# Kernel tuning notes

Hardware: AMD Instinct MI355X
Metric: run time of the kernel (lower is better)

## Reference

```python
import jax, jax.numpy as jnp
import numpy as np

_B, _Q, _D, _H, _L, _F, _C, _HM = 8, 100, 256, 8, 9, 2048, 151, 112


def setup_inputs():
    key = jax.random.key(0)
    ks = list(jax.random.split(key, 40)); ki = [0]
    def nk():
        k = ks[ki[0]]; ki[0] += 1; return k
    def r(shape, s=1.0):
        return jax.random.normal(nk(), shape, jnp.float32) * s
    z, o = jnp.zeros, jnp.ones
    return {
        'mask_features': r((_B, _D, _HM, _HM)),
        'mem0': r((_B, _D, 14, 14)), 'mem1': r((_B, _D, 28, 28)), 'mem2': r((_B, _D, 56, 56)),
        'query_feat': r((_Q, _D), 0.02), 'query_embed': r((_Q, _D), 0.02),
        'ca_wqkv': r((_L, 3, _D, _D), 0.02), 'ca_bqkv': z((_L, 3, _D)),
        'ca_wo': r((_L, _D, _D), 0.02), 'ca_bo': z((_L, _D)),
        'ca_ln_s': o((_L, _D)), 'ca_ln_b': z((_L, _D)),
        'sa_wqkv': r((_L, 3, _D, _D), 0.02), 'sa_bqkv': z((_L, 3, _D)),
        'sa_wo': r((_L, _D, _D), 0.02), 'sa_bo': z((_L, _D)),
        'sa_ln_s': o((_L, _D)), 'sa_ln_b': z((_L, _D)),
        'ffn_w1': r((_L, _D, _F), 0.02), 'ffn_b1': z((_L, _F)),
        'ffn_w2': r((_L, _F, _D), 0.02), 'ffn_b2': z((_L, _D)),
        'ffn_ln_s': o((_L, _D)), 'ffn_ln_b': z((_L, _D)),
        'dec_ln_s': o((_D,)), 'dec_ln_b': z((_D,)),
        'me_w1': r((_D, _D), 0.02), 'me_b1': z((_D,)),
        'me_w2': r((_D, _D), 0.02), 'me_b2': z((_D,)),
        'me_w3': r((_D, _D), 0.02), 'me_b3': z((_D,)),
        'cls_w': r((_D, _C), 0.02), 'cls_b': z((_C,)),
    }


def _ln(x, s, b, eps=1e-5):
    m = x.mean(-1, keepdims=True)
    v = ((x - m) ** 2).mean(-1, keepdims=True)
    return (x - m) * jax.lax.rsqrt(v + eps) * s + b


def _mha(q, k, v, wqkv, bqkv, wo, bo, bias):
    # q: [B,Nq,D]; k,v: [B,Nk,D]; bias: [B,1,Nq,Nk] additive (-1e9 = masked) or None
    B, Nq, D = q.shape
    hd = D // _H
    qh = (q @ wqkv[0] + bqkv[0]).reshape(B, Nq, _H, hd)
    kh = (k @ wqkv[1] + bqkv[1]).reshape(B, -1, _H, hd)
    vh = (v @ wqkv[2] + bqkv[2]).reshape(B, -1, _H, hd)
    scores = jnp.einsum('bqhd,bkhd->bhqk', qh, kh) / np.sqrt(hd).astype(np.float32)
    if bias is not None:
        scores = scores + bias
    attn = jax.nn.softmax(scores, axis=-1)
    out = jnp.einsum('bhqk,bkhd->bqhd', attn, vh).reshape(B, Nq, D)
    return out @ wo + bo


def _attn_bias(prev_mask, hw):
    # prev_mask: [B,Q,Hm,Wm] raw logits -> additive bias [B,1,Q,H*W]
    B, Q = prev_mask.shape[:2]
    r = jax.image.resize(prev_mask, (B, Q) + hw, 'bilinear')  # align_corners=False
    ignore = (jax.nn.sigmoid(r) < 0.5).reshape(B, Q, -1)      # True = masked out
    fully = jnp.all(ignore, axis=-1, keepdims=True)           # un-mask fully-masked rows
    ignore = jnp.where(fully, False, ignore)
    return jnp.where(ignore, jnp.float32(-1e9), jnp.float32(0.0))[:, None]


def _forward(mask_features, mem0, mem1, mem2, query_feat, query_embed,
             ca_wqkv, ca_bqkv, ca_wo, ca_bo, ca_ln_s, ca_ln_b,
             sa_wqkv, sa_bqkv, sa_wo, sa_bo, sa_ln_s, sa_ln_b,
             ffn_w1, ffn_b1, ffn_w2, ffn_b2, ffn_ln_s, ffn_ln_b,
             dec_ln_s, dec_ln_b, me_w1, me_b1, me_w2, me_b2, me_w3, me_b3,
             cls_w, cls_b):
    B, D, Hm, Wm = mask_features.shape
    Q = query_feat.shape[0]
    mems = [(m.reshape(B, D, -1).transpose(0, 2, 1), m.shape[2:]) for m in (mem0, mem1, mem2)]
    mask_flat = mask_features.reshape(B, D, -1).transpose(0, 2, 1)  # [B,Hm*Wm,D]
    q = jnp.broadcast_to((query_feat + query_embed)[None], (B, Q, D))
    prev = None
    for i in range(_L):
        mem, hw = mems[i % 3]
        bias = _attn_bias(prev, hw) if prev is not None else None
        q = _ln(q + _mha(q, mem, mem, ca_wqkv[i], ca_bqkv[i], ca_wo[i], ca_bo[i], bias), ca_ln_s[i], ca_ln_b[i])
        q = _ln(q + _mha(q, q, q, sa_wqkv[i], sa_bqkv[i], sa_wo[i], sa_bo[i], None), sa_ln_s[i], sa_ln_b[i])
        h = jax.nn.relu(q @ ffn_w1[i] + ffn_b1[i]) @ ffn_w2[i] + ffn_b2[i]
        q = _ln(q + h, ffn_ln_s[i], ffn_ln_b[i])
        nq = _ln(q, dec_ln_s, dec_ln_b)
        me = jax.nn.relu(jax.nn.relu(nq @ me_w1 + me_b1) @ me_w2 + me_b2) @ me_w3 + me_b3
        pred_mask = jnp.einsum('bqd,bpd->bqp', me, mask_flat).reshape(B, Q, Hm, Wm)
        prev = jax.lax.stop_gradient(pred_mask)
    pred_logits = nq @ cls_w + cls_b
    return pred_logits, pred_mask


def reference(mask_features, mem0, mem1, mem2, query_feat, query_embed,
              ca_wqkv, ca_bqkv, ca_wo, ca_bo, ca_ln_s, ca_ln_b,
              sa_wqkv, sa_bqkv, sa_wo, sa_bo, sa_ln_s, sa_ln_b,
              ffn_w1, ffn_b1, ffn_w2, ffn_b2, ffn_ln_s, ffn_ln_b,
              dec_ln_s, dec_ln_b, me_w1, me_b1, me_w2, me_b2, me_w3, me_b3,
              cls_w, cls_b):
    return _forward(mask_features, mem0, mem1, mem2, query_feat, query_embed,
                    ca_wqkv, ca_bqkv, ca_wo, ca_bo, ca_ln_s, ca_ln_b,
                    sa_wqkv, sa_bqkv, sa_wo, sa_bo, sa_ln_s, sa_ln_b,
                    ffn_w1, ffn_b1, ffn_w2, ffn_b2, ffn_ln_s, ffn_ln_b,
                    dec_ln_s, dec_ln_b, me_w1, me_b1, me_w2, me_b2, me_w3, me_b3,
                    cls_w, cls_b)
```

## Files before the change

kernel.cpp:

```cpp
#include <hip/hip_runtime.h>
#include <cmath>

#define B_ 8
#define Q_ 100
#define D_ 256
#define H_ 8
#define HD_ 32
#define L_ 9
#define F_ 2048
#define C_ 151
#define HM_ 112
#define PMAX_ 3136
#define KT_ 128
#define RECSZ 544

typedef __attribute__((ext_vector_type(4))) short s4v;
typedef __attribute__((ext_vector_type(8))) short s8v;
typedef __attribute__((ext_vector_type(4))) float f4v;

__device__ __forceinline__ unsigned short f2bf(float x) {
  unsigned int u = __float_as_uint(x);
  return (unsigned short)((u + 0x7fffu + ((u >> 16) & 1u)) >> 16);
}
__device__ __forceinline__ float bf2f(unsigned short h) {
  return __uint_as_float(((unsigned int)h) << 16);
}
__device__ __forceinline__ void split2(float x, short& h, short& l) {
  unsigned short hb = f2bf(x);
  float r = x - bf2f(hb);
  h = (short)hb;
  l = (short)f2bf(r);
}

__device__ __forceinline__ float block_sum(float v, float* red) {
  int t = threadIdx.x;
  red[t] = v; __syncthreads();
  for (int s = 128; s > 0; s >>= 1) {
    if (t < s) red[t] += red[t + s];
    __syncthreads();
  }
  float r = red[0]; __syncthreads();
  return r;
}

__global__ __launch_bounds__(256) void initq_kernel(const float* __restrict__ qf,
                                                    const float* __restrict__ qe,
                                                    float* __restrict__ q) {
  int idx = blockIdx.x * 256 + threadIdx.x;
  int qd = idx % (Q_ * D_);
  q[idx] = qf[qd] + qe[qd];
}

__global__ __launch_bounds__(256) void tsplit_kernel(
    const float* __restrict__ in, short* __restrict__ out,
    int K, int N, long long ibs, long long obs) {
  __shared__ float tile[32][33];
  const int z = blockIdx.z;
  const int nb = blockIdx.x * 32, kb = blockIdx.y * 32;
  const float* I = in + (size_t)z * ibs;
  short* O = out + (size_t)z * obs;
  const int t = threadIdx.x;
  {
    const int r = t >> 3, c = (t & 7) * 4;
    const int gk = kb + r;
#pragma unroll
    for (int j = 0; j < 4; ++j) {
      int gn = nb + c + j;
      tile[r][c + j] = (gk < K && gn < N) ? I[(size_t)gk * N + gn] : 0.f;
    }
  }
  __syncthreads();
  {
    const int nr = t >> 3, kc = (t & 7) * 4;
    const int gn = nb + nr;
    if (gn < N) {
#pragma unroll
      for (int j = 0; j < 4; ++j) {
        int gk = kb + kc + j;
        if (gk < K) {
          short h, l; split2(tile[kc + j][nr], h, l);
          O[(size_t)gn * 2 * K + gk] = h;
          O[(size_t)gn * 2 * K + K + gk] = l;
        }
      }
    }
  }
}

__device__ __forceinline__ s8v ldfrag(const short* p) {
  s4v lo = *(const s4v*)p;
  s4v hi = *(const s4v*)(p + 16);
  return __builtin_shufflevector(lo, hi, 0, 1, 2, 3, 4, 5, 6, 7);
}

template <int BM, int AMODE, int WMODE, bool RELU, int OUT>
__global__ __launch_bounds__(256) void mgemm_kernel(
    const void* __restrict__ Ap, const void* __restrict__ Wp,
    const float* __restrict__ bias, void* __restrict__ Cv,
    int M, int N, int K,
    long long Abs, long long Wbs, long long Cbs, int ldc, int swap) {
  constexpr int MI = BM / 32;
  __shared__ short Ah[BM * 36], Al[BM * 36], Wh[128 * 36], Wl[128 * 36];
  const int z = blockIdx.z;
  const int bx = swap ? blockIdx.y : blockIdx.x;
  const int by = swap ? blockIdx.x : blockIdx.y;
  const int n0 = bx * 128, m0 = by * BM;
  const int t = threadIdx.x;
  const int lane = t & 63;
  const int wave = t >> 6;
  const int wm = wave >> 1, wn = wave & 1;
  const int lr = lane & 15, lg = lane >> 4;
  f4v acc[MI][4];
#pragma unroll
  for (int i = 0; i < MI; ++i)
#pragma unroll
    for (int j = 0; j < 4; ++j) acc[i][j] = (f4v){0.f, 0.f, 0.f, 0.f};

  for (int k0 = 0; k0 < K; k0 += 32) {
    if (AMODE == 0) {
      const float* A = (const float*)Ap + (size_t)z * Abs;
      if (BM == 64) {
        const int arow = t >> 2;
        const int kc = (t & 3) * 8;
        float x[8];
        if (m0 + arow < M) {
          const float* ap = A + (size_t)(m0 + arow) * K + k0 + kc;
          *(f4v*)&x[0] = *(const f4v*)ap;
          *(f4v*)&x[4] = *(const f4v*)(ap + 4);
        } else {
#pragma unroll
          for (int e = 0; e < 8; ++e) x[e] = 0.f;
        }
        s4v h0, h1, l0, l1;
#pragma unroll
        for (int e = 0; e < 4; ++e) { short hh, ll; split2(x[e], hh, ll); h0[e] = hh; l0[e] = ll; }
#pragma unroll
        for (int e = 0; e < 4; ++e) { short hh, ll; split2(x[4 + e], hh, ll); h1[e] = hh; l1[e] = ll; }
        *(s4v*)&Ah[arow * 36 + kc] = h0; *(s4v*)&Ah[arow * 36 + kc + 4] = h1;
        *(s4v*)&Al[arow * 36 + kc] = l0; *(s4v*)&Al[arow * 36 + kc + 4] = l1;
      } else {
        const int arow = t >> 3;
        const int kc = (t & 7) * 4;
        float x[4];
        if (m0 + arow < M) {
          *(f4v*)&x[0] = *(const f4v*)(A + (size_t)(m0 + arow) * K + k0 + kc);
        } else {
#pragma unroll
          for (int e = 0; e < 4; ++e) x[e] = 0.f;
        }
        s4v h0, l0;
#pragma unroll
        for (int e = 0; e < 4; ++e) { short hh, ll; split2(x[e], hh, ll); h0[e] = hh; l0[e] = ll; }
        *(s4v*)&Ah[arow * 36 + kc] = h0;
        *(s4v*)&Al[arow * 36 + kc] = l0;
      }
    } else {
      const short* A2 = (const short*)Ap + (size_t)z * Abs;
      const int arow = t >> 2;
      const int c = t & 3, sel = c >> 1, ko = (c & 1) * 16;
      s8v v0 = {0, 0, 0, 0, 0, 0, 0, 0}, v1 = {0, 0, 0, 0, 0, 0, 0, 0};
      if (m0 + arow < M) {
        const short* ap = A2 + (size_t)(m0 + arow) * (2 * K) + sel * K + k0 + ko;
        v0 = *(const s8v*)ap;
        v1 = *(const s8v*)(ap + 8);
      }
      short* dst = sel ? Al : Ah;
      *(s4v*)&dst[arow * 36 + ko] = __builtin_shufflevector(v0, v0, 0, 1, 2, 3);
      *(s4v*)&dst[arow * 36 + ko + 4] = __builtin_shufflevector(v0, v0, 4, 5, 6, 7);
      *(s4v*)&dst[arow * 36 + ko + 8] = __builtin_shufflevector(v1, v1, 0, 1, 2, 3);
      *(s4v*)&dst[arow * 36 + ko + 12] = __builtin_shufflevector(v1, v1, 4, 5, 6, 7);
    }
    if (WMODE == 0) {
      const short* W2 = (const short*)Wp + (size_t)z * Wbs;
      const int n = t >> 1, sel = t & 1;
      const short* wp = W2 + (size_t)(n0 + n) * (2 * K) + sel * K + k0;
      short* dst = sel ? Wl : Wh;
#pragma unroll
      for (int j = 0; j < 4; ++j) {
        s8v v = *(const s8v*)(wp + j * 8);
        *(s4v*)&dst[n * 36 + j * 8] = __builtin_shufflevector(v, v, 0, 1, 2, 3);
        *(s4v*)&dst[n * 36 + j * 8 + 4] = __builtin_shufflevector(v, v, 4, 5, 6, 7);
      }
    } else {
      const float* W = (const float*)Wp + (size_t)z * Wbs;
      const int kr = t >> 3, c0 = (t & 7) * 16;
      const float* wp = W + (size_t)(k0 + kr) * N + n0 + c0;
      float x[16];
#pragma unroll
      for (int j = 0; j < 4; ++j) *(f4v*)&x[j * 4] = *(const f4v*)(wp + j * 4);
#pragma unroll
      for (int j = 0; j < 16; ++j) {
        short hh, ll; split2(x[j], hh, ll);
        Wh[(c0 + j) * 36 + kr] = hh;
        Wl[(c0 + j) * 36 + kr] = ll;
      }
    }
    __syncthreads();
    s8v whf[4], wlf[4];
#pragma unroll
    for (int ni = 0; ni < 4; ++ni) {
      whf[ni] = ldfrag(&Wh[(wn * 64 + ni * 16 + lr) * 36 + 4 * lg]);
      wlf[ni] = ldfrag(&Wl[(wn * 64 + ni * 16 + lr) * 36 + 4 * lg]);
    }
#pragma unroll
    for (int mi = 0; mi < MI; ++mi) {
      s8v ah = ldfrag(&Ah[(wm * (BM / 2) + mi * 16 + lr) * 36 + 4 * lg]);
      s8v al = ldfrag(&Al[(wm * (BM / 2) + mi * 16 + lr) * 36 + 4 * lg]);
#pragma unroll
      for (int ni = 0; ni < 4; ++ni) {
        acc[mi][ni] = __builtin_amdgcn_mfma_f32_16x16x32_bf16(ah, whf[ni], acc[mi][ni], 0, 0, 0);
        acc[mi][ni] = __builtin_amdgcn_mfma_f32_16x16x32_bf16(al, whf[ni], acc[mi][ni], 0, 0, 0);
        acc[mi][ni] = __builtin_amdgcn_mfma_f32_16x16x32_bf16(ah, wlf[ni], acc[mi][ni], 0, 0, 0);
      }
    }
    __syncthreads();
  }
  float* Cf = (float*)Cv + (size_t)z * Cbs;
  unsigned short* Ch = (unsigned short*)Cv + (size_t)z * Cbs;
#pragma unroll
  for (int mi = 0; mi < MI; ++mi) {
#pragma unroll
    for (int i = 0; i < 4; ++i) {
      int row = m0 + wm * (BM / 2) + mi * 16 + 4 * lg + i;
      if (row >= M) continue;
#pragma unroll
      for (int ni = 0; ni < 4; ++ni) {
        int col = n0 + wn * 64 + ni * 16 + lr;
        float v = acc[mi][ni][i] + (bias ? bias[col] : 0.f);
        if (RELU) v = fmaxf(v, 0.f);
        if (OUT == 0) Cf[(size_t)row * ldc + col] = v;
        else Ch[(size_t)row * ldc + col] = f2bf(v);
      }
    }
  }
}

__global__ __launch_bounds__(256) void maskhead_kernel(
    const float* __restrict__ q, const float* __restrict__ lns,
    const float* __restrict__ lnb, const short* __restrict__ W123,
    const float* __restrict__ b1, const float* __restrict__ b2,
    const float* __restrict__ b3,
    float* __restrict__ nqout, float* __restrict__ me3out) {
  __shared__ float Xb[16 * 264], Yb[16 * 264];
  __shared__ short Ah[16 * 36], Al[16 * 36], Wh[256 * 36], Wl[256 * 36];
  const int r0 = blockIdx.x * 16;
  const int t = threadIdx.x;
  const int lane = t & 63, w = t >> 6;
  const int lr = lane & 15, lg = lane >> 4;
#pragma unroll
  for (int rr = 0; rr < 4; ++rr) {
    int row = w * 4 + rr;
    int grow = r0 + row;
    f4v v = *((const f4v*)(q + (size_t)grow * D_) + lane);
    float sum = v[0] + v[1] + v[2] + v[3];
#pragma unroll
    for (int off = 32; off > 0; off >>= 1) sum += __shfl_xor(sum, off, 64);
    float mean = sum * (1.f / D_);
    float c0 = v[0] - mean, c1 = v[1] - mean, c2 = v[2] - mean, c3 = v[3] - mean;
    float vs = c0 * c0 + c1 * c1 + c2 * c2 + c3 * c3;
#pragma unroll
    for (int off = 32; off > 0; off >>= 1) vs += __shfl_xor(vs, off, 64);
    float inv = rsqrtf(vs * (1.f / D_) + 1e-5f);
    f4v sv = *((const f4v*)lns + lane);
    f4v bv = *((const f4v*)lnb + lane);
    f4v o;
    o[0] = c0 * inv * sv[0] + bv[0];
    o[1] = c1 * inv * sv[1] + bv[1];
    o[2] = c2 * inv * sv[2] + bv[2];
    o[3] = c3 * inv * sv[3] + bv[3];
    *(f4v*)&Xb[row * 264 + lane * 4] = o;
    *((f4v*)(nqout + (size_t)grow * D_) + lane) = o;
  }
  __syncthreads();
  float* src = Xb;
  float* dst = Yb;
  for (int s = 0; s < 3; ++s) {
    const short* Ws = W123 + (size_t)s * 131072;
    const float* bs = (s == 0) ? b1 : ((s == 1) ? b2 : b3);
    f4v acc[4];
#pragma unroll
    for (int j = 0; j < 4; ++j) acc[j] = (f4v){0.f, 0.f, 0.f, 0.f};
    for (int k0 = 0; k0 < 256; k0 += 32) {
      {
        int idx = t * 2;
        int row = idx >> 5, kc = idx & 31;
        short h0, l0, h1, l1;
        split2(src[row * 264 + k0 + kc], h0, l0);
        split2(src[row * 264 + k0 + kc + 1], h1, l1);
        Ah[row * 36 + kc] = h0; Ah[row * 36 + kc + 1] = h1;
        Al[row * 36 + kc] = l0; Al[row * 36 + kc + 1] = l1;
      }
      {
        const short* wp = Ws + (size_t)t * 512 + k0;
#pragma unroll
        for (int j = 0; j < 8; ++j)
          *(s4v*)&Wh[t * 36 + j * 4] = *(const s4v*)(wp + j * 4);
        const short* wpl = wp + 256;
#pragma unroll
        for (int j = 0; j < 8; ++j)
          *(s4v*)&Wl[t * 36 + j * 4] = *(const s4v*)(wpl + j * 4);
      }
      __syncthreads();
      s8v ah = ldfrag(&Ah[lr * 36 + 4 * lg]);
      s8v al = ldfrag(&Al[lr * 36 + 4 * lg]);
#pragma unroll
      for (int ni = 0; ni < 4; ++ni) {
        s8v wh = ldfrag(&Wh[(w * 64 + ni * 16 + lr) * 36 + 4 * lg]);
        s8v wl = ldfrag(&Wl[(w * 64 + ni * 16 + lr) * 36 + 4 * lg]);
        acc[ni] = __builtin_amdgcn_mfma_f32_16x16x32_bf16(ah, wh, acc[ni], 0, 0, 0);
        acc[ni] = __builtin_amdgcn_mfma_f32_16x16x32_bf16(al, wh, acc[ni], 0, 0, 0);
        acc[ni] = __builtin_amdgcn_mfma_f32_16x16x32_bf16(ah, wl, acc[ni], 0, 0, 0);
      }
      __syncthreads();
    }
#pragma unroll
    for (int ni = 0; ni < 4; ++ni) {
#pragma unroll
      for (int i = 0; i < 4; ++i) {
        int row = 4 * lg + i;
        int col = w * 64 + ni * 16 + lr;
        float v = acc[ni][i] + bs[col];
        if (s < 2) v = fmaxf(v, 0.f);
        dst[row * 264 + col] = v;
      }
    }
    __syncthreads();
    float* tmpp = src; src = dst; dst = tmpp;
  }
  for (int o = t; o < 16 * 256; o += 256) {
    int row = o >> 8, col = o & 255;
    me3out[(size_t)(r0 + row) * D_ + col] = src[row * 264 + col];
  }
}

__global__ __launch_bounds__(256) void gemm32_kernel(
    const float* __restrict__ A, const float* __restrict__ W,
    const float* __restrict__ bias, float* __restrict__ C,
    int M, int N, int K) {
  __shared__ float As[16][65];
  __shared__ float Ws[16][65];
  const int n0 = blockIdx.x * 64, m0 = blockIdx.y * 64;
  const int t = threadIdx.x;
  const int tm = t >> 4, tn = t & 15;
  float acc[4][4] = {};
  for (int k0 = 0; k0 < K; k0 += 16) {
#pragma unroll
    for (int l = 0; l < 4; ++l) {
      int idx = t + l * 256;
      int am = idx >> 4, ak = idx & 15;
      int gm = m0 + am, gk = k0 + ak;
      As[ak][am] = (gm < M) ? A[(size_t)gm * K + gk] : 0.f;
      int wk = idx >> 6, wn = idx & 63;
      int gn = n0 + wn, gk2 = k0 + wk;
      Ws[wk][wn] = (gn < N) ? W[(size_t)gk2 * N + gn] : 0.f;
    }
    __syncthreads();
#pragma unroll
    for (int kk = 0; kk < 16; ++kk) {
      float a[4], b[4];
#pragma unroll
      for (int i = 0; i < 4; ++i) a[i] = As[kk][tm * 4 + i];
#pragma unroll
      for (int j = 0; j < 4; ++j) b[j] = Ws[kk][tn * 4 + j];
#pragma unroll
      for (int i = 0; i < 4; ++i)
#pragma unroll
        for (int j = 0; j < 4; ++j) acc[i][j] += a[i] * b[j];
    }
    __syncthreads();
  }
#pragma unroll
  for (int i = 0; i < 4; ++i) {
    int gm = m0 + tm * 4 + i;
    if (gm >= M) continue;
#pragma unroll
    for (int j = 0; j < 4; ++j) {
      int gn = n0 + tn * 4 + j;
      if (gn >= N) continue;
      C[(size_t)gm * N + gn] = acc[i][j] + bias[gn];
    }
  }
}

template <bool RES>
__global__ __launch_bounds__(256) void ln_kernel(const float* __restrict__ x,
                                                 const float* __restrict__ r,
                                                 const float* __restrict__ s,
                                                 const float* __restrict__ b,
                                                 float* __restrict__ out, int nrows) {
  const int wave = threadIdx.x >> 6, lane = threadIdx.x & 63;
  const int row = blockIdx.x * 4 + wave;
  if (row >= nrows) return;
  f4v v = *((const f4v*)(x + (size_t)row * D_) + lane);
  if (RES) {
    f4v rv = *((const f4v*)(r + (size_t)row * D_) + lane);
    v[0] += rv[0]; v[1] += rv[1]; v[2] += rv[2]; v[3] += rv[3];
  }
  float sum = v[0] + v[1] + v[2] + v[3];
#pragma unroll
  for (int off = 32; off > 0; off >>= 1) sum += __shfl_xor(sum, off, 64);
  float mean = sum * (1.f / D_);
  float c0 = v[0] - mean, c1 = v[1] - mean, c2 = v[2] - mean, c3 = v[3] - mean;
  float vs = c0 * c0 + c1 * c1 + c2 * c2 + c3 * c3;
#pragma unroll
  for (int off = 32; off > 0; off >>= 1) vs += __shfl_xor(vs, off, 64);
  float inv = rsqrtf(vs * (1.f / D_) + 1e-5f);
  f4v sv = *((const f4v*)s + lane);
  f4v bv = *((const f4v*)b + lane);
  f4v o;
  o[0] = c0 * inv * sv[0] + bv[0];
  o[1] = c1 * inv * sv[1] + bv[1];
  o[2] = c2 * inv * sv[2] + bv[2];
  o[3] = c3 * inv * sv[3] + bv[3];
  *((f4v*)(out + (size_t)row * D_) + lane) = o;
}

template <bool BIAS, bool KVBF16, bool SPLIT>
__global__ __launch_bounds__(256) void mattn_kernel(
    const float* __restrict__ qb, int ldq,
    const void* __restrict__ kbv, int ldk,
    const void* __restrict__ vbv, int ldv,
    const unsigned int* __restrict__ bits,
    float* __restrict__ outp, int P, int Pw, int tps, int S) {
  __shared__ __align__(16) short Kt[128 * 40];
  __shared__ __align__(16) short Vt[32 * 132];
  __shared__ __align__(16) short Pt[4 * 16 * 36];
  __shared__ unsigned int bb[64];
  __shared__ float Msh[4][16], Lsh[4][16];
  float* Osh = (float*)Kt;
  const int b = blockIdx.x >> 3, h = blockIdx.x & 7;
  const int q0 = blockIdx.y * 16;
  const int seg = blockIdx.z;
  const int kbeg = seg * tps * KT_;
  const int kend = min(P, kbeg + tps * KT_);
  const int t = threadIdx.x;
  const int lane = t & 63, w = t >> 6;
  const int lr = lane & 15, lg = lane >> 4;
  const float scale = 0.17677669529663687f;

  s8v qhf, qlf;
  {
    int qrow = q0 + lr; if (qrow >= Q_) qrow = Q_ - 1;
    const float* qp = qb + (size_t)(b * Q_ + qrow) * ldq + h * HD_;
#pragma unroll
    for (int e = 0; e < 8; ++e) {
      int d = 4 * lg + (e & 3) + 16 * (e >> 2);
      short hh, ll; split2(qp[d], hh, ll);
      qhf[e] = hh; qlf[e] = ll;
    }
  }
  float mreg[4], lreg[4];
  f4v accO0 = (f4v){0.f, 0.f, 0.f, 0.f}, accO1 = (f4v){0.f, 0.f, 0.f, 0.f};
#pragma unroll
  for (int i = 0; i < 4; ++i) { mreg[i] = -3.0e38f; lreg[i] = 0.f; }

  for (int k0 = kbeg; k0 < kend; k0 += KT_) {
    {
      const int key = t >> 1, dh = (t & 1) * 16;
      const int gk = k0 + key;
      s8v ka = {0,0,0,0,0,0,0,0}, kb2 = {0,0,0,0,0,0,0,0};
      s8v va = {0,0,0,0,0,0,0,0}, vb2 = {0,0,0,0,0,0,0,0};
      if (gk < kend) {
        if (KVBF16) {
          const unsigned short* kp = (const unsigned short*)kbv + (size_t)(b * P + gk) * ldk + h * HD_ + dh;
          const unsigned short* vp = (const unsigned short*)vbv + (size_t)(b * P + gk) * ldv + h * HD_ + dh;
          ka = *(const s8v*)kp; kb2 = *(const s8v*)(kp + 8);
          va = *(const s8v*)vp; vb2 = *(const s8v*)(vp + 8);
        } else {
          const float* kp = (const float*)kbv + (size_t)(b * P + gk) * ldk + h * HD_ + dh;
          const float* vp = (const float*)vbv + (size_t)(b * P + gk) * ldv + h * HD_ + dh;
#pragma unroll
          for (int j = 0; j < 8; ++j) {
            ka[j] = (short)f2bf(kp[j]); kb2[j] = (short)f2bf(kp[8 + j]);
            va[j] = (short)f2bf(vp[j]); vb2[j] = (short)f2bf(vp[8 + j]);
          }
        }
      }
      *(s8v*)&Kt[key * 40 + dh] = ka;
      *(s8v*)&Kt[key * 40 + dh + 8] = kb2;
#pragma unroll
      for (int j = 0; j < 8; ++j) {
        Vt[(dh + j) * 132 + key] = va[j];
        Vt[(dh + 8 + j) * 132 + key] = vb2[j];
      }
    }
    if (BIAS && t < 64) {
      int qq = t >> 2, wi = t & 3;
      int gr = q0 + qq, gw = (k0 >> 5) + wi;
      bb[t] = (gr < Q_ && gw < Pw) ? bits[(size_t)(b * Q_ + gr) * Pw + gw] : 0u;
    }
    __syncthreads();
    s8v kf0 = ldfrag(&Kt[(w * 32 + lr) * 40 + 4 * lg]);
    s8v kf1 = ldfrag(&Kt[(w * 32 + 16 + lr) * 40 + 4 * lg]);
    f4v accS0 = (f4v){0.f, 0.f, 0.f, 0.f}, accS1 = (f4v){0.f, 0.f, 0.f, 0.f};
    accS0 = __builtin_amdgcn_mfma_f32_16x16x32_bf16(qhf, kf0, accS0, 0, 0, 0);
    accS0 = __builtin_amdgcn_mfma_f32_16x16x32_bf16(qlf, kf0, accS0, 0, 0, 0);
    accS1 = __builtin_amdgcn_mfma_f32_16x16x32_bf16(qhf, kf1, accS1, 0, 0, 0);
    accS1 = __builtin_amdgcn_mfma_f32_16x16x32_bf16(qlf, kf1, accS1, 0, 0, 0);
    const int gk0 = k0 + w * 32 + lr;
#pragma unroll
    for (int i = 0; i < 4; ++i) {
      float s0 = accS0[i] * scale, s1 = accS1[i] * scale;
      if (BIAS) {
        unsigned int word = bb[(4 * lg + i) * 4 + w];
        if ((word >> lr) & 1u) s0 += -1e9f;
        if ((word >> (16 + lr)) & 1u) s1 += -1e9f;
      }
      if (gk0 >= kend) s0 = -3.0e38f;
      if (gk0 + 16 >= kend) s1 = -3.0e38f;
      float rm = fmaxf(s0, s1);
#pragma unroll
      for (int off = 1; off < 16; off <<= 1) rm = fmaxf(rm, __shfl_xor(rm, off, 64));
      float mn = fmaxf(mreg[i], rm);
      float corr = __expf(mreg[i] - mn);
      mreg[i] = mn;
      float p0 = __expf(s0 - mn), p1 = __expf(s1 - mn);
      lreg[i] = lreg[i] * corr + p0 + p1;
      accO0[i] *= corr;
      accO1[i] *= corr;
      Pt[w * 576 + (4 * lg + i) * 36 + lr] = (short)f2bf(p0);
      Pt[w * 576 + (4 * lg + i) * 36 + 16 + lr] = (short)f2bf(p1);
    }
    s8v pf = ldfrag(&Pt[w * 576 + lr * 36 + 4 * lg]);
    s8v vf0 = ldfrag(&Vt[lr * 132 + w * 32 + 4 * lg]);
    s8v vf1 = ldfrag(&Vt[(16 + lr) * 132 + w * 32 + 4 * lg]);
    accO0 = __builtin_amdgcn_mfma_f32_16x16x32_bf16(pf, vf0, accO0, 0, 0, 0);
    accO1 = __builtin_amdgcn_mfma_f32_16x16x32_bf16(pf, vf1, accO1, 0, 0, 0);
    __syncthreads();
  }
#pragma unroll
  for (int i = 0; i < 4; ++i) {
    float lv = lreg[i];
#pragma unroll
    for (int off = 1; off < 16; off <<= 1) lv += __shfl_xor(lv, off, 64);
    if (lr == 0) { Msh[w][4 * lg + i] = mreg[i]; Lsh[w][4 * lg + i] = lv; }
  }
#pragma unroll
  for (int i = 0; i < 4; ++i) {
    Osh[w * 528 + (4 * lg + i) * 33 + lr] = accO0[i];
    Osh[w * 528 + (4 * lg + i) * 33 + 16 + lr] = accO1[i];
  }
  __syncthreads();
  float* part = SPLIT
      ? outp + ((size_t)((blockIdx.x * gridDim.y + blockIdx.y) * S + seg)) * RECSZ
      : nullptr;
  for (int o = t; o < 512; o += 256) {
    int qq = o >> 5, d = o & 31;
    float M = fmaxf(fmaxf(Msh[0][qq], Msh[1][qq]), fmaxf(Msh[2][qq], Msh[3][qq]));
    float lt = 0.f, Ov = 0.f;
#pragma unroll
    for (int w4 = 0; w4 < 4; ++w4) {
      float wt = __expf(Msh[w4][qq] - M);
      lt += wt * Lsh[w4][qq];
      Ov += wt * Osh[w4 * 528 + qq * 33 + d];
    }
    if (SPLIT) {
      if (d == 0) { part[qq] = M; part[16 + qq] = lt; }
      part[32 + qq * 32 + d] = Ov;
    } else if (q0 + qq < Q_) {
      outp[(size_t)(b * Q_ + q0 + qq) * D_ + h * HD_ + d] = Ov / lt;
    }
  }
}

__global__ __launch_bounds__(256) void attncomb_kernel(
    const float* __restrict__ part, float* __restrict__ out, int S, int nqt) {
  const int row = blockIdx.x;
  const int b = row / Q_, qq = row % Q_;
  const int t = threadIdx.x;
  const int h = t >> 5, d = t & 31;
  const int qt = qq >> 4, r = qq & 15;
  const float* base = part + ((size_t)((b * 8 + h) * nqt + qt) * S) * RECSZ;
  float M = -3.0e38f;
  for (int s = 0; s < S; ++s) M = fmaxf(M, base[(size_t)s * RECSZ + r]);
  float lt = 0.f, Ov = 0.f;
  for (int s = 0; s < S; ++s) {
    const float* rec = base + (size_t)s * RECSZ;
    float w = __expf(rec[r] - M);
    lt += w * rec[16 + r];
    Ov += w * rec[32 + r * 32 + d];
  }
  out[(size_t)row * D_ + h * HD_ + d] = Ov / lt;
}

__global__ __launch_bounds__(256) void maskbias_kernel(
    const float* __restrict__ prev,
    unsigned int* __restrict__ bias,
    int oh) {
  __shared__ float pm[HM_ * HM_];
  __shared__ float rbuf[PMAX_];
  __shared__ float red[256];
  __shared__ unsigned int bw[128];
  const int row = blockIdx.x;
  const int t = threadIdx.x;
  const float* src = prev + (size_t)row * (HM_ * HM_);
  for (int i = t; i < HM_ * HM_; i += 256) pm[i] = src[i];
  __syncthreads();
  const int ratio = HM_ / oh;
  const int taps = 2 * ratio;
  const float invr = 1.f / (float)ratio;
  const int P = oh * oh;
  const int Pw = (P + 31) >> 5;
  float nign = 0.f;
  for (int p = t; p < P; p += 256) {
    int oy = p / oh, ox = p - oy * oh;
    float sy = (oy + 0.5f) * ratio - 0.5f;
    float sx = (ox + 0.5f) * ratio - 0.5f;
    int y0 = (int)floorf(sy - ratio) + 1;
    int x0 = (int)floorf(sx - ratio) + 1;
    float wxs = 0.f;
    for (int si = 0; si < taps; ++si) {
      int x = x0 + si;
      if (x < 0 || x >= HM_) continue;
      wxs += 1.f - fabsf(sx - x) * invr;
    }
    float acc = 0.f, wys = 0.f;
    for (int ti = 0; ti < taps; ++ti) {
      int y = y0 + ti;
      if (y < 0 || y >= HM_) continue;
      float wy = 1.f - fabsf(sy - y) * invr;
      wys += wy;
      float ra = 0.f;
      const float* pr = pm + y * HM_;
      for (int si = 0; si < taps; ++si) {
        int x = x0 + si;
        if (x < 0 || x >= HM_) continue;
        float wx = 1.f - fabsf(sx - x) * invr;
        ra += wx * pr[x];
      }
      acc += wy * ra;
    }
    float rv = acc / (wys * wxs);
    rbuf[p] = rv;
    if (!(rv < 0.f)) nign += 1.f;
  }
  float tot = block_sum(nign, red);
  bool fully = (tot == 0.f);
  for (int w = t; w < Pw; w += 256) bw[w] = 0u;
  __syncthreads();
  if (!fully) {
    for (int p = t; p < P; p += 256) {
      if (rbuf[p] < 0.f) atomicOr(&bw[p >> 5], 1u << (p & 31));
    }
  }
  __syncthreads();
  unsigned int* dst = bias + (size_t)row * Pw;
  for (int w = t; w < Pw; w += 256) dst[w] = bw[w];
}

static inline void mg(hipStream_t st, int bm, int amode, int wmode, bool relu,
                      const void* A, const void* W, const float* bias, void* C,
                      int M, int N, int K, int Z,
                      long long Abs, long long Wbs, long long Cbs, int ldc) {
  dim3 g(N / 128, (M + bm - 1) / bm, Z);
  if (bm == 32) {
    if (relu)
      mgemm_kernel<32, 0, 0, true, 0><<<g, 256, 0, st>>>(A, W, bias, C, M, N, K, Abs, Wbs, Cbs, ldc, 0);
    else
      mgemm_kernel<32, 0, 0, false, 0><<<g, 256, 0, st>>>(A, W, bias, C, M, N, K, Abs, Wbs, Cbs, ldc, 0);
  } else {
    if (amode == 1)
      mgemm_kernel<64, 1, 0, false, 1><<<g, 256, 0, st>>>(A, W, bias, C, M, N, K, Abs, Wbs, Cbs, ldc, 0);
    else
      mgemm_kernel<64, 0, 0, false, 0><<<g, 256, 0, st>>>(A, W, bias, C, M, N, K, Abs, Wbs, Cbs, ldc, 0);
  }
}

extern "C" void kernel_launch(void* const* d_in, const int* in_sizes, int n_in,
                              void* d_out, int out_size, void* d_ws, size_t ws_size,
                              hipStream_t stream) {
  const float* mask_features = (const float*)d_in[0];
  const float* mem[3] = {(const float*)d_in[1], (const float*)d_in[2], (const float*)d_in[3]};
  const float* qf = (const float*)d_in[4];
  const float* qe = (const float*)d_in[5];
  const float* ca_wqkv = (const float*)d_in[6];
  const float* ca_bqkv = (const float*)d_in[7];
  const float* ca_wo = (const float*)d_in[8];
  const float* ca_bo = (const float*)d_in[9];
  const float* ca_ln_s = (const float*)d_in[10];
  const float* ca_ln_b = (const float*)d_in[11];
  const float* sa_wqkv = (const float*)d_in[12];
  const float* sa_bqkv = (const float*)d_in[13];
  const float* sa_wo = (const float*)d_in[14];
  const float* sa_bo = (const float*)d_in[15];
  const float* sa_ln_s = (const float*)d_in[16];
  const float* sa_ln_b = (const float*)d_in[17];
  const float* ffn_w1 = (const float*)d_in[18];
  const float* ffn_b1 = (const float*)d_in[19];
  const float* ffn_w2 = (const float*)d_in[20];
  const float* ffn_b2 = (const float*)d_in[21];
  const float* ffn_ln_s = (const float*)d_in[22];
  const float* ffn_ln_b = (const float*)d_in[23];
  const float* dec_ln_s = (const float*)d_in[24];
  const float* dec_ln_b = (const float*)d_in[25];
  const float* me_w1 = (const float*)d_in[26];
  const float* me_b1 = (const float*)d_in[27];
  const float* me_w2 = (const float*)d_in[28];
  const float* me_b2 = (const float*)d_in[29];
  const float* me_w3 = (const float*)d_in[30];
  const float* me_b3 = (const float*)d_in[31];
  const float* cls_w = (const float*)d_in[32];
  const float* cls_b = (const float*)d_in[33];

  float* out_logits = (float*)d_out;
  float* out_mask = (float*)d_out + (size_t)800 * C_;

  float* fws = (float*)d_ws;
  float* q      = fws; fws += (size_t)800 * D_;
  float* qh     = fws; fws += (size_t)800 * D_;
  float* attn_o = fws; fws += (size_t)800 * D_;
  float* tmp    = fws; fws += (size_t)800 * D_;
  float* nq     = fws; fws += (size_t)800 * D_;
  float* me3    = fws; fws += (size_t)800 * D_;
  float* kvbuf  = fws; fws += (size_t)B_ * PMAX_ * 256;
  float* qkvbuf = fws; fws += (size_t)800 * 768;
  float* biasb  = fws; fws += (size_t)800 * 128;
  float* ffnh   = fws; fws += (size_t)B_ * Q_ * F_;
  float* part   = fws; fws += (size_t)64 * 7 * 3 * RECSZ;

  unsigned short* kvb = (unsigned short*)kvbuf;
  unsigned int* biasbits = (unsigned int*)biasb;

  short* sws = (short*)fws;
  short* W2ca  = sws; sws += (size_t)27 * 256 * 512;
  short* W2sa  = sws; sws += (size_t)27 * 256 * 512;
  short* W2cao = sws; sws += (size_t)9 * 256 * 512;
  short* W2sao = sws; sws += (size_t)9 * 256 * 512;
  short* W2f1  = sws; sws += (size_t)9 * 2048 * 512;
  short* W2f2  = sws; sws += (size_t)9 * 256 * 4096;
  short* W2me  = sws; sws += (size_t)3 * 256 * 512;
  short* mem2s = sws; sws += (size_t)B_ * 3136 * 512;
  short* mem1s = sws; sws += (size_t)B_ * 784 * 512;
  short* mem0s = sws; sws += (size_t)B_ * 196 * 512;
  short* memsp[3] = {mem0s, mem1s, mem2s};

  tsplit_kernel<<<dim3(8, 8, 27), 256, 0, stream>>>(ca_wqkv, W2ca, 256, 256, 65536, 131072);
  tsplit_kernel<<<dim3(8, 8, 27), 256, 0, stream>>>(sa_wqkv, W2sa, 256, 256, 65536, 131072);
  tsplit_kernel<<<dim3(8, 8, 9), 256, 0, stream>>>(ca_wo, W2cao, 256, 256, 65536, 131072);
  tsplit_kernel<<<dim3(8, 8, 9), 256, 0, stream>>>(sa_wo, W2sao, 256, 256, 65536, 131072);
  tsplit_kernel<<<dim3(64, 8, 9), 256, 0, stream>>>(ffn_w1, W2f1, 256, 2048, 524288, 1048576);
  tsplit_kernel<<<dim3(8, 64, 9), 256, 0, stream>>>(ffn_w2, W2f2, 2048, 256, 524288, 1048576);
  tsplit_kernel<<<dim3(8, 8, 1), 256, 0, stream>>>(me_w1, W2me, 256, 256, 0, 0);
  tsplit_kernel<<<dim3(8, 8, 1), 256, 0, stream>>>(me_w2, W2me + 131072, 256, 256, 0, 0);
  tsplit_kernel<<<dim3(8, 8, 1), 256, 0, stream>>>(me_w3, W2me + 262144, 256, 256, 0, 0);
  tsplit_kernel<<<dim3(7, 8, 8), 256, 0, stream>>>(mem[0], mem0s, 256, 196, 256 * 196, 196 * 512);
  tsplit_kernel<<<dim3(25, 8, 8), 256, 0, stream>>>(mem[1], mem1s, 256, 784, 256 * 784, 784 * 512);
  tsplit_kernel<<<dim3(98, 8, 8), 256, 0, stream>>>(mem[2], mem2s, 256, 3136, 256 * 3136, 3136 * 512);

  initq_kernel<<<800, 256, 0, stream>>>(qf, qe, q);

  const int Ps[3] = {196, 784, 3136};
  const int ohs[3] = {14, 28, 56};
  const int Ss[3] = {1, 2, 3};
  for (int i = 0; i < L_; ++i) {
    const int mi = i % 3, P = Ps[mi], oh = ohs[mi];
    const int Pw = (P + 31) >> 5;
    const int S = Ss[mi];
    const int ntiles = (P + KT_ - 1) / KT_;
    const int tps = (ntiles + S - 1) / S;
    if (i > 0) maskbias_kernel<<<800, 256, 0, stream>>>(out_mask, biasbits, oh);
    mg(stream, 32, 0, 0, false, q, W2ca + (size_t)(i * 3) * 131072, ca_bqkv + i * 768, qh,
       800, 256, 256, 1, 0, 0, 0, 256);
    mg(stream, 64, 1, 0, false, memsp[mi], W2ca + (size_t)(i * 3 + 1) * 131072,
       ca_bqkv + i * 768 + 256, kvb,
       P, 512, 256, B_, (long long)P * 512, 0, (long long)P * 512, 512);
    {
      dim3 ag(64, 7, S);
      if (S > 1) {
        if (i > 0)
          mattn_kernel<true, true, true><<<ag, 256, 0, stream>>>(
              qh, 256, kvb, 512, kvb + 256, 512, biasbits, part, P, Pw, tps, S);
        else
          mattn_kernel<false, true, true><<<ag, 256, 0, stream>>>(
              qh, 256, kvb, 512, kvb + 256, 512, nullptr, part, P, Pw, tps, S);
        attncomb_kernel<<<800, 256, 0, stream>>>(part, attn_o, S, 7);
      } else {
        if (i > 0)
          mattn_kernel<true, true, false><<<ag, 256, 0, stream>>>(
              qh, 256, kvb, 512, kvb + 256, 512, biasbits, attn_o, P, Pw, tps, S);
        else
          mattn_kernel<false, true, false><<<ag, 256, 0, stream>>>(
              qh, 256, kvb, 512, kvb + 256, 512, nullptr, attn_o, P, Pw, tps, S);
      }
    }
    mg(stream, 32, 0, 0, false, attn_o, W2cao + (size_t)i * 131072, ca_bo + i * 256, tmp,
       800, 256, 256, 1, 0, 0, 0, 256);
    ln_kernel<true><<<200, 256, 0, stream>>>(tmp, q, ca_ln_s + i * 256, ca_ln_b + i * 256, q, 800);
    mg(stream, 32, 0, 0, false, q, W2sa + (size_t)(i * 3) * 131072, sa_bqkv + i * 768, qkvbuf,
       800, 768, 256, 1, 0, 0, 0, 768);
    mattn_kernel<false, false, false><<<dim3(64, 7, 1), 256, 0, stream>>>(
        qkvbuf, 768, qkvbuf + 256, 768, qkvbuf + 512, 768, nullptr, attn_o, 100, 4, 1, 1);
    mg(stream, 32, 0, 0, false, attn_o, W2sao + (size_t)i * 131072, sa_bo + i * 256, tmp,
       800, 256, 256, 1, 0, 0, 0, 256);
    ln_kernel<true><<<200, 256, 0, stream>>>(tmp, q, sa_ln_s + i * 256, sa_ln_b + i * 256, q, 800);
    mg(stream, 32, 0, 0, true, q, W2f1 + (size_t)i * 1048576, ffn_b1 + i * 2048, ffnh,
       800, 2048, 256, 1, 0, 0, 0, 2048);
    mg(stream, 32, 0, 0, false, ffnh, W2f2 + (size_t)i * 1048576, ffn_b2 + i * 256, tmp,
       800, 256, 2048, 1, 0, 0, 0, 256);
    ln_kernel<true><<<200, 256, 0, stream>>>(tmp, q, ffn_ln_s + i * 256, ffn_ln_b + i * 256, q, 800);
    maskhead_kernel<<<50, 256, 0, stream>>>(q, dec_ln_s, dec_ln_b, W2me,
                                            me_b1, me_b2, me_b3, nq, me3);
    mgemm_kernel<64, 0, 1, false, 0><<<dim3(2, 98, 8), 256, 0, stream>>>(
        me3, mask_features, nullptr, out_mask, 100, 12544, 256,
        (long long)100 * 256, (long long)256 * 12544, (long long)100 * 12544, 12544, 1);
  }
  gemm32_kernel<<<dim3(3, 13, 1), 256, 0, stream>>>(nq, cls_w, cls_b, out_logits, 800, C_, 256);
}
```

Before: 3.382 ms.

## Resize mask features once and compute attention bias at target resolution

Uses linearity of the bilinear/area resize to downsample mask_features to 14, 28 and 56 resolution once up front. Each layer's mask prediction then becomes a small GEMM against the pre-resized features, followed by a cheap bit-packing kernel. The full 112x112 mask GEMM and the per-row resize run only on the last layer. This drops most of the large mask-logit GEMM and resize work, at the cost of extra workspace and floating-point reordering that could flip the sign of values near zero.

After: 2.980 ms. 11.9% less time.

```diff
diff --git a/kernel.cpp b/kernel.cpp
--- a/kernel.cpp
+++ b/kernel.cpp
@@ -51,6 +51,50 @@
   q[idx] = qf[qd] + qe[qd];
 }
 
+__global__ __launch_bounds__(256) void resize3_kernel(
+    const float* __restrict__ mf, float* __restrict__ r0,
+    float* __restrict__ r1, float* __restrict__ r2) {
+  const int bd = blockIdx.x;
+  const float* pl = mf + (size_t)bd * (HM_ * HM_);
+  for (int pp = threadIdx.x; pp < 4116; pp += 256) {
+    int oh, p; float* out;
+    if (pp < 196)      { oh = 14; p = pp;        out = r0 + (size_t)bd * 196; }
+    else if (pp < 980) { oh = 28; p = pp - 196;  out = r1 + (size_t)bd * 784; }
+    else               { oh = 56; p = pp - 980;  out = r2 + (size_t)bd * 3136; }
+    const int ratio = HM_ / oh;
+    const int taps = 2 * ratio;
+    const float invr = 1.f / (float)ratio;
+    int oy = p / oh, ox = p - oy * oh;
+    float sy = (oy + 0.5f) * ratio - 0.5f;
+    float sx = (ox + 0.5f) * ratio - 0.5f;
+    int y0 = (int)floorf(sy - ratio) + 1;
+    int x0 = (int)floorf(sx - ratio) + 1;
+    float wxs = 0.f;
+    for (int si = 0; si < taps; ++si) {
+      int x = x0 + si;
+      if (x < 0 || x >= HM_) continue;
+      wxs += 1.f - fabsf(sx - x) * invr;
+    }
+    float acc = 0.f, wys = 0.f;
+    for (int ti = 0; ti < taps; ++ti) {
+      int y = y0 + ti;
+      if (y < 0 || y >= HM_) continue;
+      float wy = 1.f - fabsf(sy - y) * invr;
+      wys += wy;
+      float ra = 0.f;
+      const float* pr = pl + y * HM_;
+      for (int si = 0; si < taps; ++si) {
+        int x = x0 + si;
+        if (x < 0 || x >= HM_) continue;
+        float wx = 1.f - fabsf(sx - x) * invr;
+        ra += wx * pr[x];
+      }
+      acc += wy * ra;
+    }
+    out[p] = acc / (wys * wxs);
+  }
+}
+
 __global__ __launch_bounds__(256) void tsplit_kernel(
     const float* __restrict__ in, short* __restrict__ out,
     int K, int N, long long ibs, long long obs) {
@@ -74,6 +118,42 @@
     const int nr = t >> 3, kc = (t & 7) * 4;
     const int gn = nb + nr;
     if (gn < N) {
+#pragma unroll
+      for (int j = 0; j < 4; ++j) {
+        int gk = kb + kc + j;
+        if (gk < K) {
+          short h, l; split2(tile[kc + j][nr], h, l);
+          O[(size_t)gn * 2 * K + gk] = h;
+          O[(size_t)gn * 2 * K + K + gk] = l;
+        }
+      }
+    }
+  }
+}
+
+__global__ __launch_bounds__(256) void tsplitp_kernel(
+    const float* __restrict__ in, short* __restrict__ out,
+    int K, int N, int Na, long long ibs, long long obs) {
+  __shared__ float tile[32][33];
+  const int z = blockIdx.z;
+  const int nb = blockIdx.x * 32, kb = blockIdx.y * 32;
+  const float* I = in + (size_t)z * ibs;
+  short* O = out + (size_t)z * obs;
+  const int t = threadIdx.x;
+  {
+    const int r = t >> 3, c = (t & 7) * 4;
+    const int gk = kb + r;
+#pragma unroll
+    for (int j = 0; j < 4; ++j) {
+      int gn = nb + c + j;
+      tile[r][c + j] = (gk < K && gn < N) ? I[(size_t)gk * N + gn] : 0.f;
+    }
+  }
+  __syncthreads();
+  {
+    const int nr = t >> 3, kc = (t & 7) * 4;
+    const int gn = nb + nr;
+    if (gn < Na) {
 #pragma unroll
       for (int j = 0; j < 4; ++j) {
         int gk = kb + kc + j;
@@ -583,64 +663,25 @@
   out[(size_t)row * D_ + h * HD_ + d] = Ov / lt;
 }
 
-__global__ __launch_bounds__(256) void maskbias_kernel(
-    const float* __restrict__ prev,
-    unsigned int* __restrict__ bias,
-    int oh) {
-  __shared__ float pm[HM_ * HM_];
-  __shared__ float rbuf[PMAX_];
+__global__ __launch_bounds__(256) void packbits_kernel(
+    const float* __restrict__ r, unsigned int* __restrict__ bias, int P, int ldr) {
   __shared__ float red[256];
   __shared__ unsigned int bw[128];
   const int row = blockIdx.x;
+  const int b = row / Q_, qq = row % Q_;
   const int t = threadIdx.x;
-  const float* src = prev + (size_t)row * (HM_ * HM_);
-  for (int i = t; i < HM_ * HM_; i += 256) pm[i] = src[i];
-  __syncthreads();
-  const int ratio = HM_ / oh;
-  const int taps = 2 * ratio;
-  const float invr = 1.f / (float)ratio;
-  const int P = oh * oh;
+  const float* src = r + (size_t)b * Q_ * ldr + (size_t)qq * ldr;
   const int Pw = (P + 31) >> 5;
   float nign = 0.f;
-  for (int p = t; p < P; p += 256) {
-    int oy = p / oh, ox = p - oy * oh;
-    float sy = (oy + 0.5f) * ratio - 0.5f;
-    float sx = (ox + 0.5f) * ratio - 0.5f;
-    int y0 = (int)floorf(sy - ratio) + 1;
-    int x0 = (int)floorf(sx - ratio) + 1;
-    float wxs = 0.f;
-    for (int si = 0; si < taps; ++si) {
-      int x = x0 + si;
-      if (x < 0 || x >= HM_) continue;
-      wxs += 1.f - fabsf(sx - x) * invr;
-    }
-    float acc = 0.f, wys = 0.f;
-    for (int ti = 0; ti < taps; ++ti) {
-      int y = y0 + ti;
-      if (y < 0 || y >= HM_) continue;
-      float wy = 1.f - fabsf(sy - y) * invr;
-      wys += wy;
-      float ra = 0.f;
-      const float* pr = pm + y * HM_;
-      for (int si = 0; si < taps; ++si) {
-        int x = x0 + si;
-        if (x < 0 || x >= HM_) continue;
-        float wx = 1.f - fabsf(sx - x) * invr;
-        ra += wx * pr[x];
-      }
-      acc += wy * ra;
-    }
-    float rv = acc / (wys * wxs);
-    rbuf[p] = rv;
-    if (!(rv < 0.f)) nign += 1.f;
-  }
+  for (int p = t; p < P; p += 256)
+    if (!(src[p] < 0.f)) nign += 1.f;
   float tot = block_sum(nign, red);
   bool fully = (tot == 0.f);
   for (int w = t; w < Pw; w += 256) bw[w] = 0u;
   __syncthreads();
   if (!fully) {
     for (int p = t; p < P; p += 256) {
-      if (rbuf[p] < 0.f) atomicOr(&bw[p >> 5], 1u << (p & 31));
+      if (src[p] < 0.f) atomicOr(&bw[p >> 5], 1u << (p & 31));
     }
   }
   __syncthreads();
@@ -717,6 +758,10 @@
   float* biasb  = fws; fws += (size_t)800 * 128;
   float* ffnh   = fws; fws += (size_t)B_ * Q_ * F_;
   float* part   = fws; fws += (size_t)64 * 7 * 3 * RECSZ;
+  float* rmf0   = fws; fws += (size_t)B_ * 256 * 196;
+  float* rmf1   = fws; fws += (size_t)B_ * 256 * 784;
+  float* rmf2   = fws; fws += (size_t)B_ * 256 * 3136;
+  float* rbias  = fws; fws += (size_t)B_ * Q_ * 3200;
 
   unsigned short* kvb = (unsigned short*)kvbuf;
   unsigned int* biasbits = (unsigned int*)biasb;
@@ -733,6 +778,10 @@
   short* mem1s = sws; sws += (size_t)B_ * 784 * 512;
   short* mem0s = sws; sws += (size_t)B_ * 196 * 512;
   short* memsp[3] = {mem0s, mem1s, mem2s};
+  short* rmfs0 = sws; sws += (size_t)B_ * 256 * 512;
+  short* rmfs1 = sws; sws += (size_t)B_ * 896 * 512;
+  short* rmfs2 = sws; sws += (size_t)B_ * 3200 * 512;
+  short* rmfs[3] = {rmfs0, rmfs1, rmfs2};
 
   tsplit_kernel<<<dim3(8, 8, 27), 256, 0, stream>>>(ca_wqkv, W2ca, 256, 256, 65536, 131072);
   tsplit_kernel<<<dim3(8, 8, 27), 256, 0, stream>>>(sa_wqkv, W2sa, 256, 256, 65536, 131072);
@@ -747,18 +796,25 @@
   tsplit_kernel<<<dim3(25, 8, 8), 256, 0, stream>>>(mem[1], mem1s, 256, 784, 256 * 784, 784 * 512);
   tsplit_kernel<<<dim3(98, 8, 8), 256, 0, stream>>>(mem[2], mem2s, 256, 3136, 256 * 3136, 3136 * 512);
 
+  resize3_kernel<<<2048, 256, 0, stream>>>(mask_features, rmf0, rmf1, rmf2);
+  tsplitp_kernel<<<dim3(8, 8, 8), 256, 0, stream>>>(rmf0, rmfs0, 256, 196, 256,
+                                                    256 * 196, 256 * 512);
+  tsplitp_kernel<<<dim3(28, 8, 8), 256, 0, stream>>>(rmf1, rmfs1, 256, 784, 896,
+                                                     256 * 784, 896 * 512);
+  tsplitp_kernel<<<dim3(100, 8, 8), 256, 0, stream>>>(rmf2, rmfs2, 256, 3136, 3200,
+                                                      256 * 3136, 3200 * 512);
+
   initq_kernel<<<800, 256, 0, stream>>>(qf, qe, q);
 
   const int Ps[3] = {196, 784, 3136};
-  const int ohs[3] = {14, 28, 56};
+  const int Ppad[3] = {256, 896, 3200};
   const int Ss[3] = {1, 2, 3};
   for (int i = 0; i < L_; ++i) {
-    const int mi = i % 3, P = Ps[mi], oh = ohs[mi];
+    const int mi = i % 3, P = Ps[mi];
     const int Pw = (P + 31) >> 5;
     const int S = Ss[mi];
     const int ntiles = (P + KT_ - 1) / KT_;
     const int tps = (ntiles + S - 1) / S;
-    if (i > 0) maskbias_kernel<<<800, 256, 0, stream>>>(out_mask, biasbits, oh);
     mg(stream, 32, 0, 0, false, q, W2ca + (size_t)(i * 3) * 131072, ca_bqkv + i * 768, qh,
        800, 256, 256, 1, 0, 0, 0, 256);
     mg(stream, 64, 1, 0, false, memsp[mi], W2ca + (size_t)(i * 3 + 1) * 131072,
@@ -800,9 +856,18 @@
     ln_kernel<true><<<200, 256, 0, stream>>>(tmp, q, ffn_ln_s + i * 256, ffn_ln_b + i * 256, q, 800);
     maskhead_kernel<<<50, 256, 0, stream>>>(q, dec_ln_s, dec_ln_b, W2me,
                                             me_b1, me_b2, me_b3, nq, me3);
-    mgemm_kernel<64, 0, 1, false, 0><<<dim3(2, 98, 8), 256, 0, stream>>>(
-        me3, mask_features, nullptr, out_mask, 100, 12544, 256,
-        (long long)100 * 256, (long long)256 * 12544, (long long)100 * 12544, 12544, 1);
+    if (i < L_ - 1) {
+      const int mn = (i + 1) % 3;
+      const int Pn = Ps[mn], Pp = Ppad[mn];
+      mgemm_kernel<32, 0, 0, false, 0><<<dim3(Pp / 128, 4, 8), 256, 0, stream>>>(
+          me3, rmfs[mn], nullptr, rbias, 100, Pp, 256,
+          (long long)100 * 256, (long long)Pp * 512, (long long)100 * Pp, Pp, 0);
+      packbits_kernel<<<800, 256, 0, stream>>>(rbias, biasbits, Pn, Pp);
+    } else {
+      mgemm_kernel<64, 0, 1, false, 0><<<dim3(2, 98, 8), 256, 0, stream>>>(
+          me3, mask_features, nullptr, out_mask, 100, 12544, 256,
+          (long long)100 * 256, (long long)256 * 12544, (long long)100 * 12544, 12544, 1);
+    }
   }
   gemm32_kernel<<<dim3(3, 13, 1), 256, 0, stream>>>(nq, cls_w, cls_b, out_logits, 800, C_, 256);
 }
```
